# Kernel optimization log

Measured on AMD Instinct MI355X. Metric: run time of the kernel, lower is better.

Reference implementation:

```python
import jax, jax.numpy as jnp
import numpy as np

N, C, NIRR, E = 2048, 128, 9, 10          # nodes, channels, sum(2l+1) of input irreps, num elements
DOUT = (1, 3)                              # output irrep dims for 128x0e + 128x1o
K3, K2, K1 = 4, 3, 2                       # number of CG paths per correlation order


def setup_inputs() -> dict:
    key = jax.random.key(0)
    ks = jax.random.split(key, 24)
    inp = {
        'node_feats': jax.random.normal(ks[0], (N, C, NIRR), jnp.float32),
        'node_attrs': jax.nn.one_hot(jax.random.randint(ks[1], (N,), 0, E), E, dtype=jnp.float32),
        'sc': jax.random.normal(ks[2], (N, C * sum(DOUT)), jnp.float32),
    }
    i = 3
    for li, d in enumerate(DOUT):
        # U tensors: fixed (buffer) generalized CG coupling tensors; sparse in e3nn,
        # here random dense stand-ins with the exact same shapes / contraction structure.
        inp[f'u3_l{li}'] = 0.1 * jax.random.normal(ks[i + 0], (d, NIRR, NIRR, NIRR, K3), jnp.float32)
        inp[f'u2_l{li}'] = 0.1 * jax.random.normal(ks[i + 1], (d, NIRR, NIRR, K2), jnp.float32)
        inp[f'u1_l{li}'] = 0.1 * jax.random.normal(ks[i + 2], (d, NIRR, K1), jnp.float32)
        s3, s2, s1 = 1.0 / np.sqrt(K3 * C), 1.0 / np.sqrt(K2 * C), 1.0 / np.sqrt(K1 * C)
        inp[f'w3_l{li}'] = s3 * jax.random.normal(ks[i + 3], (E, K3, C), jnp.float32)
        inp[f'w2_l{li}'] = s2 * jax.random.normal(ks[i + 4], (E, K2, C), jnp.float32)
        inp[f'w1_l{li}'] = s1 * jax.random.normal(ks[i + 5], (E, K1, C), jnp.float32)
        i += 6
    inp['lin_w0'] = jax.random.normal(ks[i], (C, C), jnp.float32)
    inp['lin_w1'] = jax.random.normal(ks[i + 1], (C, C), jnp.float32)
    return inp


def _contraction(x, y, u3, u2, u1, w3, w2, w1):
    # MACE Contraction: correlation-3 nested CG contraction for one output irrep.
    # x: [N,C,n], y: [N,E] one-hot, u_nu: [d, n*nu, k_nu], w_nu: [E, k_nu, C]
    wk3 = jnp.einsum('ekc,be->bkc', w3, y)                       # per-node path weights
    out = jnp.einsum('dpqik,bkc,bci->bcdpq', u3, wk3, x)         # main, nu=3
    out = jnp.einsum('dpik,ekc,be->bcdpi', u2, w2, y) + out      # add nu=2 weights
    out = jnp.einsum('bcdpi,bci->bcdp', out, x)                  # contract one feature index
    out = jnp.einsum('dik,ekc,be->bcdi', u1, w1, y) + out        # add nu=1 weights
    out = jnp.einsum('bcdi,bci->bcd', out, x)                    # [N,C,d]
    return out


def reference(node_feats, node_attrs, sc,
              u3_l0, u2_l0, u1_l0, w3_l0, w2_l0, w1_l0,
              u3_l1, u2_l1, u1_l1, w3_l1, w2_l1, w1_l1,
              lin_w0, lin_w1):
    f0 = _contraction(node_feats, node_attrs, u3_l0, u2_l0, u1_l0, w3_l0, w2_l0, w1_l0)  # [N,C,1]
    f1 = _contraction(node_feats, node_attrs, u3_l1, u2_l1, u1_l1, w3_l1, w2_l1, w1_l1)  # [N,C,3]
    inv_sqrt_c = 1.0 / np.sqrt(C).astype(np.float32)
    # o3.Linear: block-diagonal channel mixing per irrep, 1/sqrt(fan_in) normalization
    o0 = jnp.einsum('bim,ij->bjm', f0, lin_w0) * inv_sqrt_c
    o1 = jnp.einsum('bim,ij->bjm', f1, lin_w1) * inv_sqrt_c
    out = jnp.concatenate([o0.reshape(o0.shape[0], -1), o1.reshape(o1.shape[0], -1)], axis=-1)
    return out + sc
```

## Files before the change

### kernel.cpp

```cpp
#include <hip/hip_runtime.h>

#define N_NODES 2048
#define C_CH    128
#define NIRR    9
#define E_EL    10

#define NKT 14
#define UTAB_HALVES (NKT * 512)

typedef _Float16 f16x8 __attribute__((ext_vector_type(8)));
typedef float   f32x16 __attribute__((ext_vector_type(16)));
typedef float   f32x4u __attribute__((ext_vector_type(4), aligned(4)));
typedef float   pf2    __attribute__((ext_vector_type(2)));

struct MonoTab {
    unsigned char a[224], b2[224], c[224], msk[224];
};
constexpr MonoTab makeMono() {
    MonoTab m{};
    int s3 = 0;
    for (int p = 0; p < 9; p++)
        for (int q = p; q < 9; q++)
            for (int i = q; i < 9; i++) { m.a[s3] = p; m.b2[s3] = q; m.c[s3] = i; m.msk[s3] = 1; s3++; }
    int s2 = 0;
    for (int p = 0; p < 9; p++)
        for (int q = p; q < 9; q++) { m.a[165 + s2] = p; m.b2[165 + s2] = q; m.c[165 + s2] = 9; m.msk[165 + s2] = 1; s2++; }
    for (int p = 0; p < 9; p++) { m.a[210 + p] = p; m.b2[210 + p] = 9; m.c[210 + p] = 9; m.msk[210 + p] = 1; }
    for (int k = 219; k < 224; k++) { m.a[k] = 9; m.b2[k] = 9; m.c[k] = 9; m.msk[k] = 0; }
    return m;
}
constexpr MonoTab MT = makeMono();

__global__ __launch_bounds__(256) void build_utab_kernel(
    const float* __restrict__ u3_l0, const float* __restrict__ u2_l0, const float* __restrict__ u1_l0,
    const float* __restrict__ u3_l1, const float* __restrict__ u2_l1, const float* __restrict__ u1_l1,
    _Float16* __restrict__ Utab, float* __restrict__ us1f)
{
    int t = blockIdx.x * 256 + threadIdx.x;
    if (t < UTAB_HALVES) {
        int kt = t / 512, idx = t % 512;
        int lane = idx >> 3, j = idx & 7;
        int m = lane & 31, g = lane >> 5;
        int k = kt * 16 + g * 8 + j;
        float v = 0.f;
        if (m < 16) {
            int ds = m >> 2, kk = m & 3;
            if (k < 165) {
                int pp = MT.a[k], qq = MT.b2[k], ii = MT.c[k];
                const float* u = (ds == 0) ? u3_l0 : (u3_l1 + (ds - 1) * 2916);
                int perm[6][3] = {{pp,qq,ii},{pp,ii,qq},{qq,pp,ii},{qq,ii,pp},{ii,pp,qq},{ii,qq,pp}};
                float acc = 0.f;
                #pragma unroll
                for (int w = 0; w < 6; w++)
                    acc += u[((perm[w][0] * 9 + perm[w][1]) * 9 + perm[w][2]) * 4 + kk];
                float mult = (pp == qq && qq == ii) ? 6.f : ((pp == qq || qq == ii) ? 2.f : 1.f);
                v = acc / mult;
            }
        } else if (m < 28) {
            int r = m - 16, ds = r / 3, kk = r % 3;
            if (k >= 165 && k < 210) {
                int pp = MT.a[k], qq = MT.b2[k];
                const float* u = (ds == 0) ? u2_l0 : (u2_l1 + (ds - 1) * 243);
                float acc = u[(pp * 9 + qq) * 3 + kk] + u[(qq * 9 + pp) * 3 + kk];
                v = (pp == qq) ? acc * 0.5f : acc;
            }
        } else {
            int r = m - 28, ds = r >> 1, kk = r & 1;
            if (k >= 210 && k < 219) {
                int p = k - 210;
                v = (ds == 0) ? u1_l0[p * 2 + kk] : u1_l1[(0 * 9 + p) * 2 + kk];
            }
        }
        Utab[t] = (_Float16)v;
    } else if (t < UTAB_HALVES + 72) {
        int q = t - UTAB_HALVES;
        int ds = q / 18, rem = q % 18, p = rem >> 1, kk = rem & 1;
        us1f[q] = (ds == 0) ? u1_l0[p * 2 + kk] : u1_l1[((ds - 1) * 9 + p) * 2 + kk];
    }
}

__global__ __launch_bounds__(512, 4) void fused_kernel(
    const float* __restrict__ x, const float* __restrict__ y,
    const _Float16* __restrict__ Utab, const float* __restrict__ us1f,
    const float* __restrict__ w3_l0, const float* __restrict__ w2_l0, const float* __restrict__ w1_l0,
    const float* __restrict__ w3_l1, const float* __restrict__ w2_l1, const float* __restrict__ w1_l1,
    const float* __restrict__ lw0, const float* __restrict__ lw1,
    const float* __restrict__ sc, float* __restrict__ out)
{
    __shared__ float fs[4][4][132];
    int tid = threadIdx.x;
    int lane = tid & 63;
    int wid = tid >> 6;
    int n = lane & 31, g = lane >> 5;
    int b0 = blockIdx.x * 4;
    int nd = wid >> 1;
    int b = b0 + nd;
    int th = wid & 1;

    const f16x8* U8 = (const f16x8*)Utab;

    int e = 0;
    #pragma unroll
    for (int k = 1; k < E_EL; k++)
        if (y[b * E_EL + k] > 0.5f) e = k;
    e = __builtin_amdgcn_readfirstlane(e);

    #pragma unroll 1
    for (int tl2 = 0; tl2 < 2; tl2++) {
        int c = (th * 2 + tl2) * 32 + n;
        const float* xp = x + ((size_t)b * C_CH + c) * NIRR;
        f32x4u xa = *(const f32x4u*)xp;
        f32x4u xb = *(const f32x4u*)(xp + 4);
        float xv10[10] = {xa[0], xa[1], xa[2], xa[3], xb[0], xb[1], xb[2], xb[3], xp[8], 1.f};

        f32x16 acc;
        #pragma unroll
        for (int z = 0; z < 16; z++) acc[z] = 0.f;

        #pragma unroll
        for (int kt = 0; kt < NKT; kt++) {
            f16x8 af = U8[kt * 64 + lane];
            float mf[8];
            if (g == 0) {
                #pragma unroll
                for (int j = 0; j < 8; j++) {
                    const int k = kt * 16 + j;
                    mf[j] = MT.msk[k] ? xv10[MT.a[k]] * xv10[MT.b2[k]] * xv10[MT.c[k]] : 0.f;
                }
            } else {
                #pragma unroll
                for (int j = 0; j < 8; j++) {
                    const int k = kt * 16 + 8 + j;
                    mf[j] = MT.msk[k] ? xv10[MT.a[k]] * xv10[MT.b2[k]] * xv10[MT.c[k]] : 0.f;
                }
            }
            f16x8 bf;
            #pragma unroll
            for (int j = 0; j < 8; j++) bf[j] = (_Float16)mf[j];
            acc = __builtin_amdgcn_mfma_f32_32x32x16_f16(af, bf, acc, 0, 0, 0);
        }

        float G1hi[4];
        #pragma unroll
        for (int dd = 0; dd < 2; dd++) {
            #pragma unroll
            for (int kk = 0; kk < 2; kk++) {
                float a = 0.f;
                #pragma unroll
                for (int p = 0; p < 9; p++)
                    a += us1f[(2 + dd) * 18 + p * 2 + kk] * xv10[p];
                G1hi[dd * 2 + kk] = a;
            }
        }

        float p0, p1, p2, p3;
        if (g == 0) {
            p0 = 0.f;
            #pragma unroll
            for (int kk = 0; kk < 4; kk++) p0 += w3_l0[(e * 4 + kk) * 128 + c] * acc[kk];
            #pragma unroll
            for (int kk = 0; kk < 3; kk++) p0 += w2_l0[(e * 3 + kk) * 128 + c] * acc[8 + kk];
            p1 = w2_l1[(e * 3 + 0) * 128 + c] * acc[11];
            p2 = 0.f;
            #pragma unroll
            for (int kk = 0; kk < 4; kk++) p2 += w3_l1[(e * 4 + kk) * 128 + c] * acc[4 + kk];
            p2 += w2_l1[(e * 3 + 2) * 128 + c] * acc[12];
            p3 = 0.f;
            #pragma unroll
            for (int kk = 0; kk < 3; kk++) p3 += w2_l1[(e * 3 + kk) * 128 + c] * acc[13 + kk];
            #pragma unroll
            for (int kk = 0; kk < 2; kk++) p3 += w1_l1[(e * 2 + kk) * 128 + c] * G1hi[2 + kk];
        } else {
            p0 = w1_l0[(e * 2 + 0) * 128 + c] * acc[12]
               + w1_l0[(e * 2 + 1) * 128 + c] * acc[13];
            p1 = 0.f;
            #pragma unroll
            for (int kk = 0; kk < 4; kk++) p1 += w3_l1[(e * 4 + kk) * 128 + c] * acc[kk];
            p1 += w2_l1[(e * 3 + 1) * 128 + c] * acc[8];
            p1 += w2_l1[(e * 3 + 2) * 128 + c] * acc[9];
            #pragma unroll
            for (int kk = 0; kk < 2; kk++) p1 += w1_l1[(e * 2 + kk) * 128 + c] * acc[14 + kk];
            p2 = w2_l1[(e * 3 + 0) * 128 + c] * acc[10]
               + w2_l1[(e * 3 + 1) * 128 + c] * acc[11];
            #pragma unroll
            for (int kk = 0; kk < 2; kk++) p2 += w1_l1[(e * 2 + kk) * 128 + c] * G1hi[kk];
            p3 = 0.f;
            #pragma unroll
            for (int kk = 0; kk < 4; kk++) p3 += w3_l1[(e * 4 + kk) * 128 + c] * acc[4 + kk];
        }
        float f0 = p0 + __shfl_xor(p0, 32, 64);
        float f1 = p1 + __shfl_xor(p1, 32, 64);
        float f2 = p2 + __shfl_xor(p2, 32, 64);
        float f3 = p3 + __shfl_xor(p3, 32, 64);

        if (g == 0) {
            fs[nd][0][c] = f0;
            fs[nd][1][c] = f1;
        } else {
            fs[nd][2][c] = f2;
            fs[nd][3][c] = f3;
        }
    }
    __syncthreads();

    if (tid < 256) {
        int p = tid >> 7;
        int t = tid & 127;
        int sel, m = 0, j0;
        const float4* W4;
        bool isl0 = (t < 32);
        if (isl0) { sel = 0; j0 = 4 * t; W4 = (const float4*)lw0; }
        else {
            int idx = t - 32;
            m = idx >> 5;
            j0 = 4 * (idx & 31);
            sel = 1 + m;
            W4 = (const float4*)lw1;
        }
        int wbase = j0 >> 2;

        pf2 a01A = {0.f, 0.f}, a23A = {0.f, 0.f};
        pf2 a01B = {0.f, 0.f}, a23B = {0.f, 0.f};
        #pragma unroll 4
        for (int ib = 0; ib < 32; ib++) {
            float4 fA = *(const float4*)&fs[p][sel][4 * ib];
            float4 fB = *(const float4*)&fs[p + 2][sel][4 * ib];
            float frA[4] = {fA.x, fA.y, fA.z, fA.w};
            float frB[4] = {fB.x, fB.y, fB.z, fB.w};
            #pragma unroll
            for (int r = 0; r < 4; r++) {
                float4 w = W4[(4 * ib + r) * 32 + wbase];
                pf2 wlo = {w.x, w.y};
                pf2 whi = {w.z, w.w};
                pf2 fra = {frA[r], frA[r]};
                pf2 frb = {frB[r], frB[r]};
                a01A = __builtin_elementwise_fma(wlo, fra, a01A);
                a23A = __builtin_elementwise_fma(whi, fra, a23A);
                a01B = __builtin_elementwise_fma(wlo, frb, a01B);
                a23B = __builtin_elementwise_fma(whi, frb, a23B);
            }
        }
        const float inv_sqrt_c = 0.08838834764831845f;

        {
            int bb = b0 + p;
            float a0 = a01A[0], a1 = a01A[1], a2 = a23A[0], a3 = a23A[1];
            if (isl0) {
                size_t o = (size_t)bb * 512 + j0;
                float4 s = *(const float4*)(sc + o);
                float4 rr;
                rr.x = a0 * inv_sqrt_c + s.x;
                rr.y = a1 * inv_sqrt_c + s.y;
                rr.z = a2 * inv_sqrt_c + s.z;
                rr.w = a3 * inv_sqrt_c + s.w;
                *(float4*)(out + o) = rr;
            } else {
                float av[4] = {a0, a1, a2, a3};
                #pragma unroll
                for (int jj = 0; jj < 4; jj++) {
                    size_t o = (size_t)bb * 512 + 128 + 3 * (j0 + jj) + m;
                    out[o] = av[jj] * inv_sqrt_c + sc[o];
                }
            }
        }
        {
            int bb = b0 + p + 2;
            float a0 = a01B[0], a1 = a01B[1], a2 = a23B[0], a3 = a23B[1];
            if (isl0) {
                size_t o = (size_t)bb * 512 + j0;
                float4 s = *(const float4*)(sc + o);
                float4 rr;
                rr.x = a0 * inv_sqrt_c + s.x;
                rr.y = a1 * inv_sqrt_c + s.y;
                rr.z = a2 * inv_sqrt_c + s.z;
                rr.w = a3 * inv_sqrt_c + s.w;
                *(float4*)(out + o) = rr;
            } else {
                float av[4] = {a0, a1, a2, a3};
                #pragma unroll
                for (int jj = 0; jj < 4; jj++) {
                    size_t o = (size_t)bb * 512 + 128 + 3 * (j0 + jj) + m;
                    out[o] = av[jj] * inv_sqrt_c + sc[o];
                }
            }
        }
    }
}

extern "C" void kernel_launch(void* const* d_in, const int* in_sizes, int n_in,
                              void* d_out, int out_size, void* d_ws, size_t ws_size,
                              hipStream_t stream) {
    const float* x     = (const float*)d_in[0];
    const float* y     = (const float*)d_in[1];
    const float* sc    = (const float*)d_in[2];
    const float* u3_l0 = (const float*)d_in[3];
    const float* u2_l0 = (const float*)d_in[4];
    const float* u1_l0 = (const float*)d_in[5];
    const float* w3_l0 = (const float*)d_in[6];
    const float* w2_l0 = (const float*)d_in[7];
    const float* w1_l0 = (const float*)d_in[8];
    const float* u3_l1 = (const float*)d_in[9];
    const float* u2_l1 = (const float*)d_in[10];
    const float* u1_l1 = (const float*)d_in[11];
    const float* w3_l1 = (const float*)d_in[12];
    const float* w2_l1 = (const float*)d_in[13];
    const float* w1_l1 = (const float*)d_in[14];
    const float* lw0   = (const float*)d_in[15];
    const float* lw1   = (const float*)d_in[16];
    float* out = (float*)d_out;

    _Float16* Utab = (_Float16*)d_ws;
    float* us1f = (float*)((char*)d_ws + UTAB_HALVES * 2);

    build_utab_kernel<<<(UTAB_HALVES + 72 + 255) / 256, 256, 0, stream>>>(
        u3_l0, u2_l0, u1_l0, u3_l1, u2_l1, u1_l1, Utab, us1f);
    fused_kernel<<<N_NODES / 4, 512, 0, stream>>>(
        x, y, Utab, us1f,
        w3_l0, w2_l0, w1_l0, w3_l1, w2_l1, w1_l1,
        lw0, lw1, sc, out);
}
```

Measured before the change: 117.1 us.

## Process eight nodes per block to reuse linear weights across more nodes

Each block now handles eight nodes, one wave per node covering all 128 channels in four passes, instead of four nodes with two waves each. In the final channel-mixing stage every thread accumulates four nodes per weight load instead of two, so each global read of the linear weights is reused twice as often. The cost is half as many blocks (256), more serial work per wave in the contraction phase, more shared memory and more accumulator registers. With only 256 blocks, occupancy on the GPU may drop.

```diff
diff --git a/kernel.cpp b/kernel.cpp
--- a/kernel.cpp
+++ b/kernel.cpp
@@ -87,15 +87,13 @@
     const float* __restrict__ lw0, const float* __restrict__ lw1,
     const float* __restrict__ sc, float* __restrict__ out)
 {
-    __shared__ float fs[4][4][132];
+    __shared__ float fs[8][4][132];
     int tid = threadIdx.x;
     int lane = tid & 63;
     int wid = tid >> 6;
     int n = lane & 31, g = lane >> 5;
-    int b0 = blockIdx.x * 4;
-    int nd = wid >> 1;
-    int b = b0 + nd;
-    int th = wid & 1;
+    int b0 = blockIdx.x * 8;
+    int b = b0 + wid;
 
     const f16x8* U8 = (const f16x8*)Utab;
 
@@ -106,8 +104,8 @@
     e = __builtin_amdgcn_readfirstlane(e);
 
     #pragma unroll 1
-    for (int tl2 = 0; tl2 < 2; tl2++) {
-        int c = (th * 2 + tl2) * 32 + n;
+    for (int tl = 0; tl < 4; tl++) {
+        int c = tl * 32 + n;
         const float* xp = x + ((size_t)b * C_CH + c) * NIRR;
         f32x4u xa = *(const f32x4u*)xp;
         f32x4u xb = *(const f32x4u*)(xp + 4);
@@ -194,11 +192,11 @@
         float f3 = p3 + __shfl_xor(p3, 32, 64);
 
         if (g == 0) {
-            fs[nd][0][c] = f0;
-            fs[nd][1][c] = f1;
+            fs[wid][0][c] = f0;
+            fs[wid][1][c] = f1;
         } else {
-            fs[nd][2][c] = f2;
-            fs[nd][3][c] = f3;
+            fs[wid][2][c] = f2;
+            fs[wid][3][c] = f3;
         }
     }
     __syncthreads();
@@ -219,53 +217,40 @@
         }
         int wbase = j0 >> 2;
 
-        pf2 a01A = {0.f, 0.f}, a23A = {0.f, 0.f};
-        pf2 a01B = {0.f, 0.f}, a23B = {0.f, 0.f};
+        pf2 a01[4], a23[4];
+        #pragma unroll
+        for (int k = 0; k < 4; k++) {
+            a01[k][0] = 0.f; a01[k][1] = 0.f;
+            a23[k][0] = 0.f; a23[k][1] = 0.f;
+        }
+
         #pragma unroll 4
         for (int ib = 0; ib < 32; ib++) {
-            float4 fA = *(const float4*)&fs[p][sel][4 * ib];
-            float4 fB = *(const float4*)&fs[p + 2][sel][4 * ib];
-            float frA[4] = {fA.x, fA.y, fA.z, fA.w};
-            float frB[4] = {fB.x, fB.y, fB.z, fB.w};
+            float fr[4][4];
+            #pragma unroll
+            for (int k = 0; k < 4; k++) {
+                float4 f = *(const float4*)&fs[p + 2 * k][sel][4 * ib];
+                fr[k][0] = f.x; fr[k][1] = f.y; fr[k][2] = f.z; fr[k][3] = f.w;
+            }
             #pragma unroll
             for (int r = 0; r < 4; r++) {
                 float4 w = W4[(4 * ib + r) * 32 + wbase];
                 pf2 wlo = {w.x, w.y};
                 pf2 whi = {w.z, w.w};
-                pf2 fra = {frA[r], frA[r]};
-                pf2 frb = {frB[r], frB[r]};
-                a01A = __builtin_elementwise_fma(wlo, fra, a01A);
-                a23A = __builtin_elementwise_fma(whi, fra, a23A);
-                a01B = __builtin_elementwise_fma(wlo, frb, a01B);
-                a23B = __builtin_elementwise_fma(whi, frb, a23B);
+                #pragma unroll
+                for (int k = 0; k < 4; k++) {
+                    pf2 fk = {fr[k][r], fr[k][r]};
+                    a01[k] = __builtin_elementwise_fma(wlo, fk, a01[k]);
+                    a23[k] = __builtin_elementwise_fma(whi, fk, a23[k]);
+                }
             }
         }
         const float inv_sqrt_c = 0.08838834764831845f;
 
-        {
-            int bb = b0 + p;
-            float a0 = a01A[0], a1 = a01A[1], a2 = a23A[0], a3 = a23A[1];
-            if (isl0) {
-                size_t o = (size_t)bb * 512 + j0;
-                float4 s = *(const float4*)(sc + o);
-                float4 rr;
-                rr.x = a0 * inv_sqrt_c + s.x;
-                rr.y = a1 * inv_sqrt_c + s.y;
-                rr.z = a2 * inv_sqrt_c + s.z;
-                rr.w = a3 * inv_sqrt_c + s.w;
-                *(float4*)(out + o) = rr;
-            } else {
-                float av[4] = {a0, a1, a2, a3};
-                #pragma unroll
-                for (int jj = 0; jj < 4; jj++) {
-                    size_t o = (size_t)bb * 512 + 128 + 3 * (j0 + jj) + m;
-                    out[o] = av[jj] * inv_sqrt_c + sc[o];
-                }
-            }
-        }
-        {
-            int bb = b0 + p + 2;
-            float a0 = a01B[0], a1 = a01B[1], a2 = a23B[0], a3 = a23B[1];
+        #pragma unroll
+        for (int k = 0; k < 4; k++) {
+            int bb = b0 + p + 2 * k;
+            float a0 = a01[k][0], a1 = a01[k][1], a2 = a23[k][0], a3 = a23[k][1];
             if (isl0) {
                 size_t o = (size_t)bb * 512 + j0;
                 float4 s = *(const float4*)(sc + o);
@@ -314,7 +299,7 @@
 
     build_utab_kernel<<<(UTAB_HALVES + 72 + 255) / 256, 256, 0, stream>>>(
         u3_l0, u2_l0, u1_l0, u3_l1, u2_l1, u1_l1, Utab, us1f);
-    fused_kernel<<<N_NODES / 4, 512, 0, stream>>>(
+    fused_kernel<<<N_NODES / 8, 512, 0, stream>>>(
         x, y, Utab, us1f,
         w3_l0, w2_l0, w1_l0, w3_l1, w2_l1, w1_l1,
         lw0, lw1, sc, out);
```

After: 119.7 us. 1.02x slower.
